# Kernel optimization log

Hardware: AMD Instinct MI355X
Metric: run time of the kernel (lower is better)

## Reference

```python
import jax, jax.numpy as jnp
from jax import lax
import numpy as np

B, T, D, H, OUT = 128, 1024, 256, 256, 2


def _rnn_layer(inp, W_xh, W_hh, b):
    # inp: [B, T, Din]; returns [B, T, H]
    h0 = jnp.zeros((inp.shape[0], W_hh.shape[0]), inp.dtype)

    def step(h, x_t):
        h_new = jnp.tanh(x_t @ W_xh.T + h @ W_hh.T + b)
        return h_new, h_new

    _, ys = lax.scan(step, h0, jnp.swapaxes(inp, 0, 1))  # ys: [T, B, H]
    return jnp.swapaxes(ys, 0, 1)


def setup_inputs() -> dict:
    key = jax.random.key(0)
    ks = jax.random.split(key, 8)
    s_in = 1.0 / np.sqrt(H)  # torch nn.RNN init scale
    x = jax.random.normal(ks[0], (B, T, D), dtype=jnp.float32)
    W_xh0 = jax.random.uniform(ks[1], (H, D), jnp.float32, -s_in, s_in)
    W_hh0 = jax.random.uniform(ks[2], (H, H), jnp.float32, -s_in, s_in)
    b0 = jax.random.uniform(ks[3], (H,), jnp.float32, -s_in, s_in)
    W_xh1 = jax.random.uniform(ks[4], (H, H), jnp.float32, -s_in, s_in)
    W_hh1 = jax.random.uniform(ks[5], (H, H), jnp.float32, -s_in, s_in)
    b1 = jax.random.uniform(ks[6], (H,), jnp.float32, -s_in, s_in)
    fc_w = jax.random.uniform(ks[7], (OUT, H), jnp.float32, -s_in, s_in)
    fc_b = jnp.zeros((OUT,), jnp.float32)
    return {"x": x, "W_xh0": W_xh0, "W_hh0": W_hh0, "b0": b0,
            "W_xh1": W_xh1, "W_hh1": W_hh1, "b1": b1,
            "fc_w": fc_w, "fc_b": fc_b}


def reference(x, W_xh0, W_hh0, b0, W_xh1, W_hh1, b1, fc_w, fc_b):
    h1 = _rnn_layer(x, W_xh0, W_hh0, b0)   # [B, T, H]
    h2 = _rnn_layer(h1, W_xh1, W_hh1, b1)  # [B, T, H]
    # linear head on last timestep
    return h2[:, -1, :] @ fc_w.T + fc_b    # [B, OUT]
```

## Files before the change

### kernel.cpp

```cpp
#include <hip/hip_runtime.h>

#define Bsz 128
#define Tn  1024
#define Dn  256
#define Hn  256

typedef _Float16 f16;
typedef _Float16 f16x4 __attribute__((ext_vector_type(4)));
typedef _Float16 f16x8 __attribute__((ext_vector_type(8)));
typedef float f32x4 __attribute__((ext_vector_type(4)));

__device__ __forceinline__ float tanh_fast(float x) {
    float e = __builtin_amdgcn_exp2f(x * 2.88539008177793f);
    return 1.0f - 2.0f * __builtin_amdgcn_rcpf(e + 1.0f);
}

__device__ __forceinline__ void wg_barrier() {
    asm volatile("s_waitcnt lgkmcnt(0)\n\ts_barrier" ::: "memory");
}


__global__ __launch_bounds__(256, 2) void k_xproj(
    const float* __restrict__ x, const float* __restrict__ W,
    const float* __restrict__ bias, float* __restrict__ preT)
{
    __shared__ __align__(16) f16 xt[128][264];
    const int tid = threadIdx.x;
    const int t = blockIdx.x;

    for (int i = tid; i < 128 * 64; i += 256) {
        int row = i >> 6, c4 = i & 63;
        float4 v = *(const float4*)(x + ((size_t)row * Tn + t) * Dn + c4 * 4);
        f16x4 tv = { (f16)v.x, (f16)v.y, (f16)v.z, (f16)v.w };
        *(f16x4*)(&xt[row][c4 * 4]) = tv;
    }

    const int lane = tid & 63, l15 = lane & 15, quad = lane >> 4;
    const int w = tid >> 6;

    f16x8 wf[4][8];
    #pragma unroll
    for (int jn = 0; jn < 4; jn++) {
        int j = w * 64 + jn * 16 + l15;
        #pragma unroll
        for (int kk = 0; kk < 8; kk++)
            #pragma unroll
            for (int e = 0; e < 8; e++)
                wf[jn][kk][e] = (f16)W[(size_t)j * Dn + kk * 32 + quad * 8 + e];
    }
    float4 bi[4];
    #pragma unroll
    for (int jn = 0; jn < 4; jn++)
        bi[jn] = *(const float4*)(bias + w * 64 + jn * 16 + quad * 4);

    __syncthreads();

    #pragma unroll 1
    for (int bblk = 0; bblk < 8; bblk++) {
        f32x4 acc[4];
        #pragma unroll
        for (int jn = 0; jn < 4; jn++)
            acc[jn] = (f32x4){bi[jn].x, bi[jn].y, bi[jn].z, bi[jn].w};
        #pragma unroll
        for (int kk = 0; kk < 8; kk++) {
            f16x8 xb = *(const f16x8*)(&xt[bblk * 16 + l15][kk * 32 + quad * 8]);
            #pragma unroll
            for (int jn = 0; jn < 4; jn++)
                acc[jn] = __builtin_amdgcn_mfma_f32_16x16x32_f16(wf[jn][kk], xb, acc[jn], 0, 0, 0);
        }
        #pragma unroll
        for (int jn = 0; jn < 4; jn++)
            #pragma unroll
            for (int r = 0; r < 4; r++) {
                int j = w * 64 + jn * 16 + quad * 4 + r;
                preT[((size_t)t * Hn + j) * Bsz + bblk * 16 + l15] = acc[jn][r];
            }
    }
}

__global__ __launch_bounds__(512, 2) void k_fused(
    const float* __restrict__ Whh0, const float* __restrict__ Wxh1,
    const float* __restrict__ Whh1, const float* __restrict__ b1v,
    const float* __restrict__ fcw,  const float* __restrict__ fcb,
    const float* __restrict__ preT, float* __restrict__ out)
{
    __shared__ __align__(16) f16 h1f[2][4096];
    __shared__ __align__(16) f16 h2f[2][4096];

    const int tid  = threadIdx.x;
    const int lane = tid & 63, l15 = lane & 15, quad = lane >> 4;
    const int w    = tid >> 6;
    const int colbase = w * 32;
    const int bg   = blockIdx.x * 16;

    for (int i = tid; i < 4096; i += 512) {
        h1f[0][i] = (f16)0.0f; h1f[1][i] = (f16)0.0f;
        h2f[0][i] = (f16)0.0f; h2f[1][i] = (f16)0.0f;
    }

    f16x8 wh0[2][8], wx[2][8], wh1[2][8];
    #pragma unroll
    for (int jn = 0; jn < 2; jn++) {
        int j = colbase + jn * 16 + l15;
        #pragma unroll
        for (int kk = 0; kk < 8; kk++)
            #pragma unroll
            for (int e = 0; e < 8; e++) {
                int o = (int)((size_t)j * Hn + kk * 32 + quad * 8 + e);
                wh0[jn][kk][e] = (f16)Whh0[o];
                wx [jn][kk][e] = (f16)Wxh1[o];
                wh1[jn][kk][e] = (f16)Whh1[o];
            }
    }
    float4 bi[2];
    #pragma unroll
    for (int jn = 0; jn < 2; jn++)
        bi[jn] = *(const float4*)(b1v + colbase + jn * 16 + quad * 4);

    int wroff[2];
    #pragma unroll
    for (int jn = 0; jn < 2; jn++) {
        int n0 = colbase + jn * 16 + quad * 4;
        wroff[jn] = (n0 >> 5) * 512 + ((n0 >> 3) & 3) * 128 + l15 * 8 + (n0 & 7);
    }

    float pn[8];
    #pragma unroll
    for (int jn = 0; jn < 2; jn++)
        #pragma unroll
        for (int r = 0; r < 4; r++) {
            int j = colbase + jn * 16 + quad * 4 + r;
            pn[jn * 4 + r] = preT[((size_t)0 * Hn + j) * Bsz + bg + l15];
        }
    __syncthreads();

#define FSTEP(P, TT) { \
     \
    f32x4 accA[2]; \
    _Pragma("unroll") for (int jn = 0; jn < 2; jn++) \
        _Pragma("unroll") for (int r = 0; r < 4; r++) accA[jn][r] = pn[jn*4+r]; \
    { int tf = ((TT) + 1 < Tn) ? (TT) + 1 : Tn - 1; \
      _Pragma("unroll") for (int jn = 0; jn < 2; jn++) \
          _Pragma("unroll") for (int r = 0; r < 4; r++) { \
              int j = colbase + jn * 16 + quad * 4 + r; \
              pn[jn*4+r] = preT[((size_t)tf * Hn + j) * Bsz + bg + l15]; } } \
    _Pragma("unroll") for (int kk = 0; kk < 8; kk++) { \
        f16x8 hb = *(const f16x8*)(&h1f[P][kk * 512 + lane * 8]); \
        accA[0] = __builtin_amdgcn_mfma_f32_16x16x32_f16(wh0[0][kk], hb, accA[0], 0, 0, 0); \
        accA[1] = __builtin_amdgcn_mfma_f32_16x16x32_f16(wh0[1][kk], hb, accA[1], 0, 0, 0); \
    } \
    _Pragma("unroll") for (int jn = 0; jn < 2; jn++) { \
        f16x4 t4 = { (f16)tanh_fast(accA[jn][0]), (f16)tanh_fast(accA[jn][1]), \
                     (f16)tanh_fast(accA[jn][2]), (f16)tanh_fast(accA[jn][3]) }; \
        *(f16x4*)(&h1f[1-(P)][wroff[jn]]) = t4; \
    } \
    wg_barrier();  \
     \
    f32x4 accB[2]; \
    _Pragma("unroll") for (int jn = 0; jn < 2; jn++) \
        accB[jn] = (f32x4){bi[jn].x, bi[jn].y, bi[jn].z, bi[jn].w}; \
    _Pragma("unroll") for (int kk = 0; kk < 8; kk++) { \
        f16x8 h1b = *(const f16x8*)(&h1f[1-(P)][kk * 512 + lane * 8]); \
        f16x8 h2b = *(const f16x8*)(&h2f[P][kk * 512 + lane * 8]); \
        accB[0] = __builtin_amdgcn_mfma_f32_16x16x32_f16(wx [0][kk], h1b, accB[0], 0, 0, 0); \
        accB[1] = __builtin_amdgcn_mfma_f32_16x16x32_f16(wx [1][kk], h1b, accB[1], 0, 0, 0); \
        accB[0] = __builtin_amdgcn_mfma_f32_16x16x32_f16(wh1[0][kk], h2b, accB[0], 0, 0, 0); \
        accB[1] = __builtin_amdgcn_mfma_f32_16x16x32_f16(wh1[1][kk], h2b, accB[1], 0, 0, 0); \
    } \
    _Pragma("unroll") for (int jn = 0; jn < 2; jn++) { \
        f16x4 t4 = { (f16)tanh_fast(accB[jn][0]), (f16)tanh_fast(accB[jn][1]), \
                     (f16)tanh_fast(accB[jn][2]), (f16)tanh_fast(accB[jn][3]) }; \
        *(f16x4*)(&h2f[1-(P)][wroff[jn]]) = t4; \
    } \
    wg_barrier();  \
}

    #pragma unroll 1
    for (int tp = 0; tp < Tn / 2; ++tp) {
        const int t0 = tp * 2;
        FSTEP(0, t0)
        FSTEP(1, (t0 + 1))
    }
#undef FSTEP

    if (tid < 256) {
        const int bl = tid >> 4, o = (tid >> 3) & 1, kc = tid & 7;
        float s = 0.f;
        #pragma unroll
        for (int kq = 0; kq < 32; kq++) {
            int k = kc * 32 + kq;
            f16 hv = h2f[0][(k >> 5) * 512 + ((k >> 3) & 3) * 128 + bl * 8 + (k & 7)];
            s += (float)hv * fcw[o * Hn + k];
        }
        s += __shfl_down(s, 4);
        s += __shfl_down(s, 2);
        s += __shfl_down(s, 1);
        if (kc == 0)
            out[(bg + bl) * 2 + o] = s + fcb[o];
    }
}

extern "C" void kernel_launch(void* const* d_in, const int* in_sizes, int n_in,
                              void* d_out, int out_size, void* d_ws, size_t ws_size,
                              hipStream_t stream) {
    const float* x    = (const float*)d_in[0];
    const float* Wxh0 = (const float*)d_in[1];
    const float* Whh0 = (const float*)d_in[2];
    const float* b0   = (const float*)d_in[3];
    const float* Wxh1 = (const float*)d_in[4];
    const float* Whh1 = (const float*)d_in[5];
    const float* b1   = (const float*)d_in[6];
    const float* fcw  = (const float*)d_in[7];
    const float* fcb  = (const float*)d_in[8];
    float* out = (float*)d_out;

    float* preT = (float*)d_ws;

    k_xproj<<<dim3(Tn),       dim3(256), 0, stream>>>(x, Wxh0, b0, preT);
    k_fused<<<dim3(Bsz / 16), dim3(512), 0, stream>>>(Whh0, Wxh1, Whh1, b1,
                                                      fcw, fcb, preT, out);
}
```

Before: 1.537 ms.

## Split RNN layers into pipelined producer/consumer blocks synced by global flags

The fused recurrence kernel becomes 16 blocks: 8 compute layer-0 and write h1 per timestep to global memory, then publish a per-tile progress flag. The other 8 spin on that flag and compute layer-1 from the published h1. This halves the serial per-step work in each block and pipelines the two layers across CUs. The x-projection now stores f16 in a packed layout, and each block handles 4 timesteps. The cost is global-memory round trips, spin-waiting, and relaxed-atomic ordering. It also relies on all 16 blocks being co-resident.

```diff
diff --git a/kernel.cpp b/kernel.cpp
--- a/kernel.cpp
+++ b/kernel.cpp
@@ -10,6 +10,9 @@
 typedef _Float16 f16x8 __attribute__((ext_vector_type(8)));
 typedef float f32x4 __attribute__((ext_vector_type(4)));
 
+union U8  { unsigned long long u;    f16x4 v; };
+union U16 { unsigned long long u[2]; f16x8 v; };
+
 __device__ __forceinline__ float tanh_fast(float x) {
     float e = __builtin_amdgcn_exp2f(x * 2.88539008177793f);
     return 1.0f - 2.0f * __builtin_amdgcn_rcpf(e + 1.0f);
@@ -18,104 +21,97 @@
 __device__ __forceinline__ void wg_barrier() {
     asm volatile("s_waitcnt lgkmcnt(0)\n\ts_barrier" ::: "memory");
 }
-
+__device__ __forceinline__ void full_barrier() {
+    asm volatile("s_waitcnt vmcnt(0) lgkmcnt(0)\n\ts_barrier" ::: "memory");
+}
+
+__device__ __forceinline__ size_t preB_off(int t, int j0, int b) {
+    return ((size_t)t * 64 + (j0 >> 2)) * 512 + (size_t)b * 4;
+}
 
 __global__ __launch_bounds__(256, 2) void k_xproj(
     const float* __restrict__ x, const float* __restrict__ W,
-    const float* __restrict__ bias, float* __restrict__ preT)
+    const float* __restrict__ bias, f16* __restrict__ preB,
+    unsigned int* __restrict__ flags)
 {
     __shared__ __align__(16) f16 xt[128][264];
     const int tid = threadIdx.x;
-    const int t = blockIdx.x;
-
-    for (int i = tid; i < 128 * 64; i += 256) {
-        int row = i >> 6, c4 = i & 63;
-        float4 v = *(const float4*)(x + ((size_t)row * Tn + t) * Dn + c4 * 4);
-        f16x4 tv = { (f16)v.x, (f16)v.y, (f16)v.z, (f16)v.w };
-        *(f16x4*)(&xt[row][c4 * 4]) = tv;
-    }
+    if (blockIdx.x == 0 && tid < 8) flags[tid] = 0u;
 
     const int lane = tid & 63, l15 = lane & 15, quad = lane >> 4;
-    const int w = tid >> 6;
+    const int wbase = (tid >> 6) * 64;
 
     f16x8 wf[4][8];
+    float4 bi[4];
     #pragma unroll
     for (int jn = 0; jn < 4; jn++) {
-        int j = w * 64 + jn * 16 + l15;
+        int j = wbase + jn * 16 + l15;
         #pragma unroll
         for (int kk = 0; kk < 8; kk++)
             #pragma unroll
             for (int e = 0; e < 8; e++)
                 wf[jn][kk][e] = (f16)W[(size_t)j * Dn + kk * 32 + quad * 8 + e];
     }
-    float4 bi[4];
     #pragma unroll
     for (int jn = 0; jn < 4; jn++)
-        bi[jn] = *(const float4*)(bias + w * 64 + jn * 16 + quad * 4);
-
-    __syncthreads();
+        bi[jn] = *(const float4*)(bias + wbase + jn * 16 + quad * 4);
 
     #pragma unroll 1
-    for (int bblk = 0; bblk < 8; bblk++) {
-        f32x4 acc[4];
-        #pragma unroll
-        for (int jn = 0; jn < 4; jn++)
-            acc[jn] = (f32x4){bi[jn].x, bi[jn].y, bi[jn].z, bi[jn].w};
-        #pragma unroll
-        for (int kk = 0; kk < 8; kk++) {
-            f16x8 xb = *(const f16x8*)(&xt[bblk * 16 + l15][kk * 32 + quad * 8]);
+    for (int tt = 0; tt < 4; tt++) {
+        const int t = blockIdx.x * 4 + tt;
+        __syncthreads();
+        for (int i = tid; i < 128 * 64; i += 256) {
+            int row = i >> 6, c4 = i & 63;
+            float4 v = *(const float4*)(x + ((size_t)row * Tn + t) * Dn + c4 * 4);
+            f16x4 tv = { (f16)v.x, (f16)v.y, (f16)v.z, (f16)v.w };
+            *(f16x4*)(&xt[row][c4 * 4]) = tv;
+        }
+        __syncthreads();
+
+        #pragma unroll 1
+        for (int bblk = 0; bblk < 8; bblk++) {
+            f32x4 acc[4];
             #pragma unroll
             for (int jn = 0; jn < 4; jn++)
-                acc[jn] = __builtin_amdgcn_mfma_f32_16x16x32_f16(wf[jn][kk], xb, acc[jn], 0, 0, 0);
-        }
-        #pragma unroll
-        for (int jn = 0; jn < 4; jn++)
-            #pragma unroll
-            for (int r = 0; r < 4; r++) {
-                int j = w * 64 + jn * 16 + quad * 4 + r;
-                preT[((size_t)t * Hn + j) * Bsz + bblk * 16 + l15] = acc[jn][r];
+                acc[jn] = (f32x4){bi[jn].x, bi[jn].y, bi[jn].z, bi[jn].w};
+            #pragma unroll
+            for (int kk = 0; kk < 8; kk++) {
+                f16x8 xb = *(const f16x8*)(&xt[bblk * 16 + l15][kk * 32 + quad * 8]);
+                #pragma unroll
+                for (int jn = 0; jn < 4; jn++)
+                    acc[jn] = __builtin_amdgcn_mfma_f32_16x16x32_f16(wf[jn][kk], xb, acc[jn], 0, 0, 0);
             }
-    }
-}
-
-__global__ __launch_bounds__(512, 2) void k_fused(
+            #pragma unroll
+            for (int jn = 0; jn < 4; jn++) {
+                int j0 = wbase + jn * 16 + quad * 4;
+                f16x4 pv = { (f16)acc[jn][0], (f16)acc[jn][1],
+                             (f16)acc[jn][2], (f16)acc[jn][3] };
+                *(f16x4*)(preB + preB_off(t, j0, bblk * 16 + l15)) = pv;
+            }
+        }
+    }
+}
+
+__global__ __launch_bounds__(512, 2) void k_rec(
     const float* __restrict__ Whh0, const float* __restrict__ Wxh1,
     const float* __restrict__ Whh1, const float* __restrict__ b1v,
     const float* __restrict__ fcw,  const float* __restrict__ fcb,
-    const float* __restrict__ preT, float* __restrict__ out)
+    const f16* __restrict__ preB,   f16* __restrict__ h1g,
+    unsigned int* __restrict__ flags, float* __restrict__ out)
 {
     __shared__ __align__(16) f16 h1f[2][4096];
     __shared__ __align__(16) f16 h2f[2][4096];
 
     const int tid  = threadIdx.x;
     const int lane = tid & 63, l15 = lane & 15, quad = lane >> 4;
-    const int w    = tid >> 6;
-    const int colbase = w * 32;
-    const int bg   = blockIdx.x * 16;
+    const int colbase = (tid >> 6) * 32;
+    const int stage = blockIdx.x >> 3, tile = blockIdx.x & 7;
+    const int bg = tile * 16;
 
     for (int i = tid; i < 4096; i += 512) {
         h1f[0][i] = (f16)0.0f; h1f[1][i] = (f16)0.0f;
         h2f[0][i] = (f16)0.0f; h2f[1][i] = (f16)0.0f;
     }
-
-    f16x8 wh0[2][8], wx[2][8], wh1[2][8];
-    #pragma unroll
-    for (int jn = 0; jn < 2; jn++) {
-        int j = colbase + jn * 16 + l15;
-        #pragma unroll
-        for (int kk = 0; kk < 8; kk++)
-            #pragma unroll
-            for (int e = 0; e < 8; e++) {
-                int o = (int)((size_t)j * Hn + kk * 32 + quad * 8 + e);
-                wh0[jn][kk][e] = (f16)Whh0[o];
-                wx [jn][kk][e] = (f16)Wxh1[o];
-                wh1[jn][kk][e] = (f16)Whh1[o];
-            }
-    }
-    float4 bi[2];
-    #pragma unroll
-    for (int jn = 0; jn < 2; jn++)
-        bi[jn] = *(const float4*)(b1v + colbase + jn * 16 + quad * 4);
 
     int wroff[2];
     #pragma unroll
@@ -124,79 +120,135 @@
         wroff[jn] = (n0 >> 5) * 512 + ((n0 >> 3) & 3) * 128 + l15 * 8 + (n0 & 7);
     }
 
-    float pn[8];
-    #pragma unroll
-    for (int jn = 0; jn < 2; jn++)
-        #pragma unroll
-        for (int r = 0; r < 4; r++) {
-            int j = colbase + jn * 16 + quad * 4 + r;
-            pn[jn * 4 + r] = preT[((size_t)0 * Hn + j) * Bsz + bg + l15];
-        }
-    __syncthreads();
-
-#define FSTEP(P, TT) { \
-     \
+    if (stage == 0) {
+        f16x8 wh0[2][8];
+        #pragma unroll
+        for (int jn = 0; jn < 2; jn++) {
+            int j = colbase + jn * 16 + l15;
+            #pragma unroll
+            for (int kk = 0; kk < 8; kk++)
+                #pragma unroll
+                for (int e = 0; e < 8; e++)
+                    wh0[jn][kk][e] = (f16)Whh0[(size_t)j * Hn + kk * 32 + quad * 8 + e];
+        }
+        unsigned long long* gbase = (unsigned long long*)(h1g + (size_t)tile * Tn * 4096);
+        unsigned int* flagp = flags + tile;
+
+        f16x4 pnv[2];
+        #pragma unroll
+        for (int jn = 0; jn < 2; jn++)
+            pnv[jn] = *(const f16x4*)(preB + preB_off(0, colbase + jn * 16 + quad * 4, bg + l15));
+        __syncthreads();
+
+#define S0STEP(P, TT) { \
     f32x4 accA[2]; \
     _Pragma("unroll") for (int jn = 0; jn < 2; jn++) \
-        _Pragma("unroll") for (int r = 0; r < 4; r++) accA[jn][r] = pn[jn*4+r]; \
+        _Pragma("unroll") for (int r = 0; r < 4; r++) accA[jn][r] = (float)pnv[jn][r]; \
     { int tf = ((TT) + 1 < Tn) ? (TT) + 1 : Tn - 1; \
       _Pragma("unroll") for (int jn = 0; jn < 2; jn++) \
-          _Pragma("unroll") for (int r = 0; r < 4; r++) { \
-              int j = colbase + jn * 16 + quad * 4 + r; \
-              pn[jn*4+r] = preT[((size_t)tf * Hn + j) * Bsz + bg + l15]; } } \
+          pnv[jn] = *(const f16x4*)(preB + preB_off(tf, colbase + jn * 16 + quad * 4, bg + l15)); } \
     _Pragma("unroll") for (int kk = 0; kk < 8; kk++) { \
         f16x8 hb = *(const f16x8*)(&h1f[P][kk * 512 + lane * 8]); \
         accA[0] = __builtin_amdgcn_mfma_f32_16x16x32_f16(wh0[0][kk], hb, accA[0], 0, 0, 0); \
         accA[1] = __builtin_amdgcn_mfma_f32_16x16x32_f16(wh0[1][kk], hb, accA[1], 0, 0, 0); \
     } \
+    unsigned long long* gp = gbase + (size_t)(TT) * 1024; \
     _Pragma("unroll") for (int jn = 0; jn < 2; jn++) { \
         f16x4 t4 = { (f16)tanh_fast(accA[jn][0]), (f16)tanh_fast(accA[jn][1]), \
                      (f16)tanh_fast(accA[jn][2]), (f16)tanh_fast(accA[jn][3]) }; \
         *(f16x4*)(&h1f[1-(P)][wroff[jn]]) = t4; \
-    } \
-    wg_barrier();  \
-     \
+        U8 uu; uu.v = t4; \
+        __hip_atomic_store(gp + (wroff[jn] >> 2), uu.u, __ATOMIC_RELAXED, __HIP_MEMORY_SCOPE_AGENT); \
+    } \
+    full_barrier(); \
+    if (tid == 0) \
+        __hip_atomic_store(flagp, (unsigned)(TT) + 1u, __ATOMIC_RELAXED, __HIP_MEMORY_SCOPE_AGENT); \
+}
+        #pragma unroll 1
+        for (int tp = 0; tp < Tn / 2; ++tp) {
+            const int t0 = tp * 2;
+            S0STEP(0, t0)
+            S0STEP(1, (t0 + 1))
+        }
+#undef S0STEP
+    } else {
+        f16x8 wx[2][8], wh1[2][8];
+        #pragma unroll
+        for (int jn = 0; jn < 2; jn++) {
+            int j = colbase + jn * 16 + l15;
+            #pragma unroll
+            for (int kk = 0; kk < 8; kk++)
+                #pragma unroll
+                for (int e = 0; e < 8; e++) {
+                    size_t o = (size_t)j * Hn + kk * 32 + quad * 8 + e;
+                    wx [jn][kk][e] = (f16)Wxh1[o];
+                    wh1[jn][kk][e] = (f16)Whh1[o];
+                }
+        }
+        float4 bi[2];
+        #pragma unroll
+        for (int jn = 0; jn < 2; jn++)
+            bi[jn] = *(const float4*)(b1v + colbase + jn * 16 + quad * 4);
+
+        const unsigned long long* gbase =
+            (const unsigned long long*)(h1g + (size_t)tile * Tn * 4096);
+        unsigned int* flagp = flags + tile;
+        unsigned int fl = 0u;
+        __syncthreads();
+
+#define S1STEP(Q, TT) { \
+    unsigned int need = (unsigned)(TT) + 1u; \
+    while (fl < need) \
+        fl = __hip_atomic_load(flagp, __ATOMIC_RELAXED, __HIP_MEMORY_SCOPE_AGENT); \
+    const unsigned long long* gp = gbase + (size_t)(TT) * 1024; \
+    U16 hf[8]; \
+    _Pragma("unroll") for (int kk = 0; kk < 8; kk++) { \
+        hf[kk].u[0] = __hip_atomic_load(gp + kk * 128 + lane * 2,     __ATOMIC_RELAXED, __HIP_MEMORY_SCOPE_AGENT); \
+        hf[kk].u[1] = __hip_atomic_load(gp + kk * 128 + lane * 2 + 1, __ATOMIC_RELAXED, __HIP_MEMORY_SCOPE_AGENT); \
+    } \
     f32x4 accB[2]; \
     _Pragma("unroll") for (int jn = 0; jn < 2; jn++) \
         accB[jn] = (f32x4){bi[jn].x, bi[jn].y, bi[jn].z, bi[jn].w}; \
     _Pragma("unroll") for (int kk = 0; kk < 8; kk++) { \
-        f16x8 h1b = *(const f16x8*)(&h1f[1-(P)][kk * 512 + lane * 8]); \
-        f16x8 h2b = *(const f16x8*)(&h2f[P][kk * 512 + lane * 8]); \
-        accB[0] = __builtin_amdgcn_mfma_f32_16x16x32_f16(wx [0][kk], h1b, accB[0], 0, 0, 0); \
-        accB[1] = __builtin_amdgcn_mfma_f32_16x16x32_f16(wx [1][kk], h1b, accB[1], 0, 0, 0); \
+        f16x8 h2b = *(const f16x8*)(&h2f[Q][kk * 512 + lane * 8]); \
         accB[0] = __builtin_amdgcn_mfma_f32_16x16x32_f16(wh1[0][kk], h2b, accB[0], 0, 0, 0); \
         accB[1] = __builtin_amdgcn_mfma_f32_16x16x32_f16(wh1[1][kk], h2b, accB[1], 0, 0, 0); \
     } \
+    _Pragma("unroll") for (int kk = 0; kk < 8; kk++) { \
+        accB[0] = __builtin_amdgcn_mfma_f32_16x16x32_f16(wx[0][kk], hf[kk].v, accB[0], 0, 0, 0); \
+        accB[1] = __builtin_amdgcn_mfma_f32_16x16x32_f16(wx[1][kk], hf[kk].v, accB[1], 0, 0, 0); \
+    } \
+    fl = __hip_atomic_load(flagp, __ATOMIC_RELAXED, __HIP_MEMORY_SCOPE_AGENT);  \
     _Pragma("unroll") for (int jn = 0; jn < 2; jn++) { \
         f16x4 t4 = { (f16)tanh_fast(accB[jn][0]), (f16)tanh_fast(accB[jn][1]), \
                      (f16)tanh_fast(accB[jn][2]), (f16)tanh_fast(accB[jn][3]) }; \
-        *(f16x4*)(&h2f[1-(P)][wroff[jn]]) = t4; \
-    } \
-    wg_barrier();  \
-}
-
-    #pragma unroll 1
-    for (int tp = 0; tp < Tn / 2; ++tp) {
-        const int t0 = tp * 2;
-        FSTEP(0, t0)
-        FSTEP(1, (t0 + 1))
-    }
-#undef FSTEP
-
-    if (tid < 256) {
-        const int bl = tid >> 4, o = (tid >> 3) & 1, kc = tid & 7;
-        float s = 0.f;
-        #pragma unroll
-        for (int kq = 0; kq < 32; kq++) {
-            int k = kc * 32 + kq;
-            f16 hv = h2f[0][(k >> 5) * 512 + ((k >> 3) & 3) * 128 + bl * 8 + (k & 7)];
-            s += (float)hv * fcw[o * Hn + k];
-        }
-        s += __shfl_down(s, 4);
-        s += __shfl_down(s, 2);
-        s += __shfl_down(s, 1);
-        if (kc == 0)
-            out[(bg + bl) * 2 + o] = s + fcb[o];
+        *(f16x4*)(&h2f[1-(Q)][wroff[jn]]) = t4; \
+    } \
+    wg_barrier(); \
+}
+        #pragma unroll 1
+        for (int tp = 0; tp < Tn / 2; ++tp) {
+            const int t0 = tp * 2;
+            S1STEP(0, t0)
+            S1STEP(1, (t0 + 1))
+        }
+#undef S1STEP
+
+        if (tid < 256) {
+            const int bl = tid >> 4, o = (tid >> 3) & 1, kc = tid & 7;
+            float s = 0.f;
+            #pragma unroll
+            for (int kq = 0; kq < 32; kq++) {
+                int k = kc * 32 + kq;
+                f16 hv = h2f[0][(k >> 5) * 512 + ((k >> 3) & 3) * 128 + bl * 8 + (k & 7)];
+                s += (float)hv * fcw[o * Hn + k];
+            }
+            s += __shfl_down(s, 4);
+            s += __shfl_down(s, 2);
+            s += __shfl_down(s, 1);
+            if (kc == 0)
+                out[(bg + bl) * 2 + o] = s + fcb[o];
+        }
     }
 }
 
@@ -214,9 +266,11 @@
     const float* fcb  = (const float*)d_in[8];
     float* out = (float*)d_out;
 
-    float* preT = (float*)d_ws;
-
-    k_xproj<<<dim3(Tn),       dim3(256), 0, stream>>>(x, Wxh0, b0, preT);
-    k_fused<<<dim3(Bsz / 16), dim3(512), 0, stream>>>(Whh0, Wxh1, Whh1, b1,
-                                                      fcw, fcb, preT, out);
-}
+    f16* preB = (f16*)d_ws;
+    f16* h1g  = (f16*)((char*)d_ws + ((size_t)64 << 20));
+    unsigned int* flags = (unsigned int*)((char*)d_ws + ((size_t)128 << 20));
+
+    k_xproj<<<dim3(Tn / 4), dim3(256), 0, stream>>>(x, Wxh0, b0, preB, flags);
+    k_rec  <<<dim3(16),     dim3(512), 0, stream>>>(Whh0, Wxh1, Whh1, b1,
+                                                    fcw, fcb, preB, h1g, flags, out);
+}
```

Result: slower. 2.039 ms (+32.6%).
